# Kernel optimization log

Hardware: AMD Instinct MI355X
Metric: run time of the kernel (lower is better)

The kernel has to match this reference:

```python
import jax, jax.numpy as jnp
import numpy as np

B, T, DE, DR, H = 8192, 8, 512, 1024, 1024


def setup_inputs() -> dict:
    key = jax.random.key(0)
    ks = jax.random.split(key, 8)
    std = 1.0 / np.sqrt(H)
    u = lambda k, shape: jax.random.uniform(k, shape, jnp.float32, -std, std)
    return {
        "entity": jax.random.normal(ks[0], (B, T, DE), jnp.float32),
        "relation": jax.random.normal(ks[1], (B, T, DR), jnp.float32),
        "We": u(ks[2], (H, DE)),
        "be": u(ks[3], (H,)),
        "Wr": u(ks[4], (H, DR)),
        "br": u(ks[5], (H,)),
        "Wh": u(ks[6], (H, H)),
        "bh": u(ks[7], (H,)),
    }


def reference(entity, relation, We, be, Wr, br, Wh, bh):
    # entity: [B, T, DE], relation: [B, T, DR]
    # Precompute time-parallel input projections (linear, math-equivalent to per-step).
    g = (jnp.einsum("btd,hd->bth", entity, We) + be
         + jnp.einsum("btd,hd->bth", relation, Wr) + br)  # [B, T, H]

    def step(h, gt):
        h = jax.nn.relu(gt + h @ Wh.T + bh)  # RNNCell_rel: relu(e2h(e)+r2h(r)+h2h(h))
        return h, h

    h0 = jnp.zeros((entity.shape[0], Wh.shape[0]), entity.dtype)
    hn, outs = jax.lax.scan(step, h0, jnp.transpose(g, (1, 0, 2)))  # outs: [T, B, H]
    output = jnp.transpose(outs, (1, 0, 2))  # [B, T, H] (batch-first)
    need = hn.T  # faithful to hidden[0].transpose(0,1): [H, B]
    return output, need
```

## Files before the change

### kernel.cpp

```cpp
#include <hip/hip_runtime.h>
#include <hip/hip_bf16.h>

#define BB 8192
#define TT 8
#define DEe 512
#define DRr 1024
#define HH 1024
#define KG 1536
#define MG 65536

typedef __attribute__((ext_vector_type(8))) __bf16 bf16x8;
typedef __attribute__((ext_vector_type(4))) __bf16 bf16x4;
typedef __attribute__((ext_vector_type(4))) float f32x4;

__device__ __forceinline__ void gld_lds16(const __bf16* g, __bf16* l) {
    __builtin_amdgcn_global_load_lds(
        (const __attribute__((address_space(1))) void*)g,
        (__attribute__((address_space(3))) void*)l, 16, 0, 0);
}

__global__ void pack_ga(const float* __restrict__ ent, const float* __restrict__ rel,
                        __bf16* __restrict__ ga) {
    const int total = MG * (KG / 4);
    const int stride = gridDim.x * blockDim.x;
    for (int g = blockIdx.x * blockDim.x + threadIdx.x; g < total; g += stride) {
        int m = g / 384;
        int c4 = g - m * 384;
        float4 v;
        if (c4 < 128) v = ((const float4*)ent)[(size_t)m * 128 + c4];
        else          v = ((const float4*)rel)[(size_t)m * 256 + (c4 - 128)];
        bf16x4 o = {(__bf16)v.x, (__bf16)v.y, (__bf16)v.z, (__bf16)v.w};
        *(bf16x4*)(ga + (size_t)m * KG + c4 * 4) = o;
    }
}

__global__ void pack_bw(const float* __restrict__ We, const float* __restrict__ Wr,
                        const float* __restrict__ Wh,
                        __bf16* __restrict__ BW, __bf16* __restrict__ WhT) {
    const int n = blockIdx.y;
    const int sec = blockIdx.x;
    const int i = threadIdx.x;
    float4 v; __bf16* dst;
    if (sec == 0) {
        v = *(const float4*)(We + (size_t)n * DEe + i * 4);
        dst = BW + (size_t)n * KG + i * 4;
    } else if (sec <= 2) {
        int d = (sec - 1) * 512 + i * 4;
        v = *(const float4*)(Wr + (size_t)n * DRr + d);
        dst = BW + (size_t)n * KG + DEe + d;
    } else {
        int d = (sec - 3) * 512 + i * 4;
        v = *(const float4*)(Wh + (size_t)n * HH + d);
        dst = WhT + (d >> 5) * 32768 + ((d >> 3) & 3) * 8192 + n * 8 + (d & 7);
    }
    bf16x4 o = {(__bf16)v.x, (__bf16)v.y, (__bf16)v.z, (__bf16)v.w};
    *(bf16x4*)dst = o;
}

__global__ __launch_bounds__(256) void gemm_g(
    const __bf16* __restrict__ A, const __bf16* __restrict__ Bw,
    const float* __restrict__ be, const float* __restrict__ br,
    const float* __restrict__ bh, float* __restrict__ out) {
    __shared__ __bf16 sA[128 * 32];
    __shared__ __bf16 sB[128 * 32];
    __shared__ float sBias[128];

    const int tid  = threadIdx.x;
    const int lane = tid & 63;
    const int w    = tid >> 6;
    const int bid  = blockIdx.y * 8 + blockIdx.x;
    const int swz  = (bid & 7) * 512 + (bid >> 3);
    const int tileN = (swz & 7) * 128;
    const int tileM = (swz >> 3) * 128;

    if (tid < 128) {
        int n = tileN + tid;
        sBias[tid] = be[n] + br[n] + bh[n];
    }

    const int r0 = (w * 2 + 0) * 16 + (lane >> 2);
    const int r1 = (w * 2 + 1) * 16 + (lane >> 2);
    const int cc = (lane & 3) * 8;
    const __bf16* gA0 = A + (size_t)(tileM + r0) * KG + cc;
    const __bf16* gA1 = A + (size_t)(tileM + r1) * KG + cc;
    const __bf16* gB0 = Bw + (size_t)(tileN + r0) * KG + cc;
    const __bf16* gB1 = Bw + (size_t)(tileN + r1) * KG + cc;
    __bf16* lA0 = sA + (w * 2 + 0) * 512;
    __bf16* lA1 = sA + (w * 2 + 1) * 512;
    __bf16* lB0 = sB + (w * 2 + 0) * 512;
    __bf16* lB1 = sB + (w * 2 + 1) * 512;

    const int wm = (w >> 1) * 64, wn = (w & 1) * 64;
    const int fm = lane & 15, fq = lane >> 4;

    f32x4 acc[4][4];
#pragma unroll
    for (int i = 0; i < 4; i++)
#pragma unroll
        for (int j = 0; j < 4; j++) acc[i][j] = {0.f, 0.f, 0.f, 0.f};

    for (int k0 = 0; k0 < KG; k0 += 32) {
        gld_lds16(gA0 + k0, lA0);
        gld_lds16(gA1 + k0, lA1);
        gld_lds16(gB0 + k0, lB0);
        gld_lds16(gB1 + k0, lB1);
        __syncthreads();
        bf16x8 af[4], bfv[4];
#pragma unroll
        for (int mf = 0; mf < 4; mf++)
            af[mf] = *(const bf16x8*)&sA[(wm + mf * 16 + fm) * 32 + fq * 8];
#pragma unroll
        for (int nf = 0; nf < 4; nf++)
            bfv[nf] = *(const bf16x8*)&sB[(wn + nf * 16 + fm) * 32 + fq * 8];
#pragma unroll
        for (int mf = 0; mf < 4; mf++)
#pragma unroll
            for (int nf = 0; nf < 4; nf++)
                acc[mf][nf] = __builtin_amdgcn_mfma_f32_16x16x32_bf16(
                    af[mf], bfv[nf], acc[mf][nf], 0, 0, 0);
        __syncthreads();
    }

#pragma unroll
    for (int mf = 0; mf < 4; mf++) {
#pragma unroll
        for (int nf = 0; nf < 4; nf++) {
            f32x4 v = acc[mf][nf];
            const int nl = wn + nf * 16 + fm;
            const int n  = tileN + nl;
            const int m0 = tileM + wm + mf * 16 + fq * 4;
            const float bias = sBias[nl];
            const bool t0row = ((m0 & 7) == 0);
#pragma unroll
            for (int r = 0; r < 4; r++) {
                float x = v[r] + bias;
                size_t m = (size_t)(m0 + r);
                if (t0row && r == 0) {
                    out[m * HH + n] = x > 0.f ? x : 0.f;
                } else {
                    out[m * HH + n] = x;
                }
            }
        }
    }
}

__global__ __launch_bounds__(512, 1) void rnn_local(
    const __bf16* __restrict__ Bw,
    float* __restrict__ out, float* __restrict__ need) {
    __shared__ __bf16 sH[32 * 1024];
    __shared__ __bf16 sB[32 * 1024];

    const int tid  = threadIdx.x;
    const int lane = tid & 63;
    const int w    = tid >> 6;
    const int b0   = blockIdx.x * 32;
    const int fm   = lane & 15, fq = lane >> 4;
    const int wn   = w * 128;

#pragma unroll
    for (int i = 0; i < 8; i++) {
        int c  = i * 512 + tid;
        int m  = c >> 7;
        int cc = (c & 127) * 8;
        const float* src = out + ((size_t)(b0 + m) * TT + 0) * HH + cc;
        float4 v0 = *(const float4*)src;
        float4 v1 = *(const float4*)(src + 4);
        bf16x8 o = {(__bf16)v0.x, (__bf16)v0.y, (__bf16)v0.z, (__bf16)v0.w,
                    (__bf16)v1.x, (__bf16)v1.y, (__bf16)v1.z, (__bf16)v1.w};
        int byte = (m * 2048 + cc * 2) ^ ((m & 7) << 4);
        *(bf16x8*)((char*)sH + byte) = o;
    }
    __syncthreads();

    for (int t = 1; t < TT; t++) {
        f32x4 acc[2][8];
#pragma unroll
        for (int i = 0; i < 2; i++)
#pragma unroll
            for (int j = 0; j < 8; j++) acc[i][j] = {0.f, 0.f, 0.f, 0.f};

        for (int k0i = 0; k0i < 32; k0i++) {
            const __bf16* gsrc = Bw + (size_t)k0i * 32768;
            float4 stg[8];
#pragma unroll
            for (int j = 0; j < 8; j++)
                stg[j] = *(const float4*)(gsrc + ((size_t)(j * 512 + tid)) * 8);
#pragma unroll
            for (int j = 0; j < 8; j++)
                *(float4*)(sB + (size_t)(j * 512 + tid) * 8) = stg[j];
            __syncthreads();

            bf16x8 af[2], bfv[8];
            const int kb = k0i * 64;
#pragma unroll
            for (int mf = 0; mf < 2; mf++) {
                int m = mf * 16 + fm;
                int byte = (m * 2048 + kb + fq * 16) ^ ((m & 7) << 4);
                af[mf] = *(const bf16x8*)((const char*)sH + byte);
            }
#pragma unroll
            for (int nf = 0; nf < 8; nf++) {
                int n = wn + nf * 16 + fm;
                bfv[nf] = *(const bf16x8*)((const char*)sB + (fq * 1024 + n) * 16);
            }
#pragma unroll
            for (int mf = 0; mf < 2; mf++)
#pragma unroll
                for (int nf = 0; nf < 8; nf++)
                    acc[mf][nf] = __builtin_amdgcn_mfma_f32_16x16x32_bf16(
                        af[mf], bfv[nf], acc[mf][nf], 0, 0, 0);
            __syncthreads();
        }

#pragma unroll
        for (int mf = 0; mf < 2; mf++) {
#pragma unroll
            for (int nf = 0; nf < 8; nf++) {
                f32x4 v = acc[mf][nf];
                const int n  = wn + nf * 16 + fm;
                const int m0 = mf * 16 + fq * 4;
                float hv[4];
#pragma unroll
                for (int r = 0; r < 4; r++) {
                    int m = m0 + r;
                    size_t addr = ((size_t)(b0 + m) * TT + t) * HH + n;
                    float x = v[r] + out[addr];
                    hv[r] = x > 0.f ? x : 0.f;
                    out[addr] = hv[r];
                    int byte = (m * 2048 + n * 2) ^ ((m & 7) << 4);
                    *(__bf16*)((char*)sH + byte) = (__bf16)hv[r];
                }
                if (t == 7) {
                    f32x4 nv = {hv[0], hv[1], hv[2], hv[3]};
                    *(f32x4*)&need[(size_t)n * BB + b0 + m0] = nv;
                }
            }
        }
        __syncthreads();
    }
}

extern "C" void kernel_launch(void* const* d_in, const int* in_sizes, int n_in,
                              void* d_out, int out_size, void* d_ws, size_t ws_size,
                              hipStream_t stream) {
    const float* ent = (const float*)d_in[0];
    const float* rel = (const float*)d_in[1];
    const float* We  = (const float*)d_in[2];
    const float* be  = (const float*)d_in[3];
    const float* Wr  = (const float*)d_in[4];
    const float* br  = (const float*)d_in[5];
    const float* Wh  = (const float*)d_in[6];
    const float* bh  = (const float*)d_in[7];

    float* out  = (float*)d_out;
    float* need = out + (size_t)BB * TT * HH;

    char* ws = (char*)d_ws;
    __bf16* GA  = (__bf16*)ws;
    __bf16* BW  = (__bf16*)(ws + (size_t)MG * KG * 2);
    __bf16* WhT = (__bf16*)(ws + (size_t)MG * KG * 2 + (size_t)HH * KG * 2);

    pack_bw<<<dim3(5, 1024), 128, 0, stream>>>(We, Wr, Wh, BW, WhT);
    pack_ga<<<dim3(2048), 256, 0, stream>>>(ent, rel, GA);
    gemm_g<<<dim3(8, 512), 256, 0, stream>>>(GA, BW, be, br, bh, out);
    rnn_local<<<dim3(256), dim3(512), 0, stream>>>(WhT, out, need);
}
```

Before: 1.209 ms.

## Load recurrent weights directly into registers with double-buffered prefetch, drop LDS staging

```diff
diff --git a/kernel.cpp b/kernel.cpp
--- a/kernel.cpp
+++ b/kernel.cpp
@@ -149,7 +149,6 @@
     const __bf16* __restrict__ Bw,
     float* __restrict__ out, float* __restrict__ need) {
     __shared__ __bf16 sH[32 * 1024];
-    __shared__ __bf16 sB[32 * 1024];
 
     const int tid  = threadIdx.x;
     const int lane = tid & 63;
@@ -173,6 +172,8 @@
     }
     __syncthreads();
 
+    const __bf16* bb = Bw + (size_t)fq * 8192 + (size_t)(wn + fm) * 8;
+
     for (int t = 1; t < TT; t++) {
         f32x4 acc[2][8];
 #pragma unroll
@@ -180,38 +181,45 @@
 #pragma unroll
             for (int j = 0; j < 8; j++) acc[i][j] = {0.f, 0.f, 0.f, 0.f};
 
-        for (int k0i = 0; k0i < 32; k0i++) {
-            const __bf16* gsrc = Bw + (size_t)k0i * 32768;
-            float4 stg[8];
-#pragma unroll
-            for (int j = 0; j < 8; j++)
-                stg[j] = *(const float4*)(gsrc + ((size_t)(j * 512 + tid)) * 8);
-#pragma unroll
-            for (int j = 0; j < 8; j++)
-                *(float4*)(sB + (size_t)(j * 512 + tid) * 8) = stg[j];
-            __syncthreads();
-
-            bf16x8 af[2], bfv[8];
-            const int kb = k0i * 64;
+        bf16x8 bv0[8], bv1[8];
+#pragma unroll
+        for (int nf = 0; nf < 8; nf++) bv0[nf] = *(const bf16x8*)(bb + nf * 128);
+#pragma unroll
+        for (int nf = 0; nf < 8; nf++) bv1[nf] = *(const bf16x8*)(bb + 32768 + nf * 128);
+
+        for (int k = 0; k < 32; k += 2) {
+            bf16x8 af0[2], af1[2];
 #pragma unroll
             for (int mf = 0; mf < 2; mf++) {
                 int m = mf * 16 + fm;
-                int byte = (m * 2048 + kb + fq * 16) ^ ((m & 7) << 4);
-                af[mf] = *(const bf16x8*)((const char*)sH + byte);
-            }
-#pragma unroll
-            for (int nf = 0; nf < 8; nf++) {
-                int n = wn + nf * 16 + fm;
-                bfv[nf] = *(const bf16x8*)((const char*)sB + (fq * 1024 + n) * 16);
+                int row = m * 2048, sw = (m & 7) << 4;
+                af0[mf] = *(const bf16x8*)((const char*)sH + ((row + k * 64 + fq * 16) ^ sw));
+                af1[mf] = *(const bf16x8*)((const char*)sH + ((row + (k + 1) * 64 + fq * 16) ^ sw));
             }
 #pragma unroll
             for (int mf = 0; mf < 2; mf++)
 #pragma unroll
                 for (int nf = 0; nf < 8; nf++)
                     acc[mf][nf] = __builtin_amdgcn_mfma_f32_16x16x32_bf16(
-                        af[mf], bfv[nf], acc[mf][nf], 0, 0, 0);
-            __syncthreads();
+                        af0[mf], bv0[nf], acc[mf][nf], 0, 0, 0);
+            if (k + 2 < 32) {
+                const __bf16* p = bb + (size_t)(k + 2) * 32768;
+#pragma unroll
+                for (int nf = 0; nf < 8; nf++) bv0[nf] = *(const bf16x8*)(p + nf * 128);
+            }
+#pragma unroll
+            for (int mf = 0; mf < 2; mf++)
+#pragma unroll
+                for (int nf = 0; nf < 8; nf++)
+                    acc[mf][nf] = __builtin_amdgcn_mfma_f32_16x16x32_bf16(
+                        af1[mf], bv1[nf], acc[mf][nf], 0, 0, 0);
+            if (k + 3 < 32) {
+                const __bf16* p = bb + (size_t)(k + 3) * 32768;
+#pragma unroll
+                for (int nf = 0; nf < 8; nf++) bv1[nf] = *(const bf16x8*)(p + nf * 128);
+            }
         }
+        __syncthreads();
 
 #pragma unroll
         for (int mf = 0; mf < 2; mf++) {
@@ -262,7 +270,7 @@
     __bf16* WhT = (__bf16*)(ws + (size_t)MG * KG * 2 + (size_t)HH * KG * 2);
 
     pack_bw<<<dim3(5, 1024), 128, 0, stream>>>(We, Wr, Wh, BW, WhT);
-    pack_ga<<<dim3(2048), 256, 0, stream>>>(ent, rel, GA);
+    pack_ga<<<dim3(4096), 256, 0, stream>>>(ent, rel, GA);
     gemm_g<<<dim3(8, 512), 256, 0, stream>>>(GA, BW, be, br, bh, out);
     rnn_local<<<dim3(256), dim3(512), 0, stream>>>(WhT, out, need);
 }
```

Result: slower. 2.202 ms (+82.1%).
